# Performance work log

Measured on AMD Instinct MI355X. Metric: run time of the kernel, lower is better.

## Reference

```python
import jax, jax.numpy as jnp
import numpy as np

B, S, DIM = 4, 1024, 2048
N_HEAD, N_KV, HEAD_DIM = 32, 8, 64


def setup_inputs() -> dict:
    key = jax.random.key(0)
    k1, k2, k3, k4 = jax.random.split(key, 4)
    x = jax.random.normal(k1, (B, S, DIM), dtype=jnp.float32)
    # rotary table: [S, head_dim//2, 2] = (cos, sin)
    inv_freq = 1.0 / (10000.0 ** (jnp.arange(0, HEAD_DIM, 2, dtype=jnp.float32) / HEAD_DIM))
    t = jnp.arange(S, dtype=jnp.float32)
    ang = t[:, None] * inv_freq[None, :]
    freqs_cis = jnp.stack([jnp.cos(ang), jnp.sin(ang)], axis=-1)
    mask = jnp.tril(jnp.ones((S, S), dtype=bool))[None, None]  # causal bool [1,1,S,S]
    scale = 0.02
    wqkv = jax.random.normal(k2, ((N_HEAD + 2 * N_KV) * HEAD_DIM, DIM), dtype=jnp.float32) * scale
    wo = jax.random.normal(k3, (DIM, DIM), dtype=jnp.float32) * scale
    return {"x": x, "freqs_cis": freqs_cis, "mask": mask, "wqkv": wqkv, "wo": wo}


def _apply_rotary(x, freqs_cis):
    # x: [b, s, h, d]; freqs_cis: [s, d//2, 2]
    b, s, h, d = x.shape
    xr = x.reshape(b, s, h, d // 2, 2)
    fc = freqs_cis.reshape(1, s, 1, d // 2, 2)
    cos, sin = fc[..., 0], fc[..., 1]
    x0, x1 = xr[..., 0], xr[..., 1]
    out = jnp.stack([x0 * cos - x1 * sin, x1 * cos + x0 * sin], axis=-1)
    return out.reshape(b, s, h, d)


def reference(x, freqs_cis, mask, wqkv, wo):
    b, s, _ = x.shape
    qkv = jnp.einsum('bsd,ed->bse', x, wqkv)
    q, k, v = jnp.split(qkv, [N_HEAD * HEAD_DIM, (N_HEAD + N_KV) * HEAD_DIM], axis=-1)
    q = q.reshape(b, s, N_HEAD, HEAD_DIM)
    k = k.reshape(b, s, N_KV, HEAD_DIM)
    v = v.reshape(b, s, N_KV, HEAD_DIM)
    q = _apply_rotary(q, freqs_cis)
    k = _apply_rotary(k, freqs_cis)
    # [b, h, s, d]
    q = q.transpose(0, 2, 1, 3)
    k = k.transpose(0, 2, 1, 3)
    v = v.transpose(0, 2, 1, 3)
    g = N_HEAD // N_KV
    k = jnp.repeat(k, g, axis=1)
    v = jnp.repeat(v, g, axis=1)
    scale = 1.0 / np.sqrt(HEAD_DIM).astype(np.float32)
    scores = jnp.einsum('bhqd,bhkd->bhqk', q, k) * scale
    scores = jnp.where(mask, scores, jnp.float32(-jnp.inf))
    attn = jax.nn.softmax(scores, axis=-1)
    y = jnp.einsum('bhqk,bhkd->bhqd', attn, v)
    y = y.transpose(0, 2, 1, 3).reshape(b, s, DIM)
    return jnp.einsum('bsd,ed->bse', y, wo)
```

## Files before the change

kernel.cpp:

```cpp
#include <hip/hip_runtime.h>
#include <stdint.h>

typedef __bf16 bf16;
typedef __attribute__((ext_vector_type(8))) __bf16 bf16x8;
typedef __attribute__((ext_vector_type(4))) __bf16 bf16x4;
typedef __attribute__((ext_vector_type(4))) float f32x4;
typedef __attribute__((ext_vector_type(16))) float f32x16;
typedef __attribute__((ext_vector_type(2))) unsigned u32x2;

#define AS1 __attribute__((address_space(1)))
#define AS3 __attribute__((address_space(3)))

#if __has_builtin(__builtin_amdgcn_permlane32_swap)
#define HAVE_PLSWAP 1
#else
#define HAVE_PLSWAP 0
#endif

__device__ __forceinline__ float ex2(float x) {
#if __has_builtin(__builtin_amdgcn_exp2f)
  return __builtin_amdgcn_exp2f(x);
#else
  return exp2f(x);
#endif
}

__device__ __forceinline__ void barrier_f() {
  asm volatile("" ::: "memory");
  __builtin_amdgcn_s_barrier();
  asm volatile("" ::: "memory");
}

template <int N>
__device__ __forceinline__ void waitVm() {
  if constexpr (N == 0) asm volatile("s_waitcnt vmcnt(0)" ::: "memory");
  else if constexpr (N == 1) asm volatile("s_waitcnt vmcnt(1)" ::: "memory");
  else if constexpr (N == 2) asm volatile("s_waitcnt vmcnt(2)" ::: "memory");
  else if constexpr (N == 4) asm volatile("s_waitcnt vmcnt(4)" ::: "memory");
  else if constexpr (N == 6) asm volatile("s_waitcnt vmcnt(6)" ::: "memory");
  else static_assert(N == 0, "unsupported vmcnt");
  __builtin_amdgcn_sched_barrier(0);
}

__device__ __forceinline__ u32x2 swap32(uint32_t a, uint32_t b, int hh) {
#if HAVE_PLSWAP
  (void)hh;
  return __builtin_amdgcn_permlane32_swap(a, b, false, false);
#else
  u32x2 r;
  r[0] = hh ? __shfl_xor(b, 32) : a;
  r[1] = hh ? b : __shfl_xor(a, 32);
  return r;
#endif
}

template <int K>
__device__ __forceinline__ void relay_body(const float* __restrict__ W,
                                           bf16* __restrict__ Bp, int t) {
  const int off = t * 8;
  const int sub = (off & 511) >> 3;
  const int n = sub & 15, khi = sub >> 4;
  const int blk = off >> 9;
  const int kblk = blk & ((K >> 5) - 1);
  const int nblk = blk >> (31 - __builtin_clz(K >> 5));
  const float* src = W + (size_t)(nblk * 16 + n) * K + kblk * 32 + khi * 8;
  float4 a = *reinterpret_cast<const float4*>(src);
  float4 b = *reinterpret_cast<const float4*>(src + 4);
  bf16x8 o = { (bf16)a.x, (bf16)a.y, (bf16)a.z, (bf16)a.w,
               (bf16)b.x, (bf16)b.y, (bf16)b.z, (bf16)b.w };
  *reinterpret_cast<bf16x8*>(Bp + off) = o;
}

__global__ __launch_bounds__(256) void prologue_kernel(
    const float* __restrict__ x, bf16* __restrict__ xb,
    const float* __restrict__ wqkv, bf16* __restrict__ BpQ,
    const float* __restrict__ wo, bf16* __restrict__ BpO) {
  const int blk = blockIdx.x;
  if (blk < 8192) {
    const int i = blk * 256 + threadIdx.x;
    float4 v = reinterpret_cast<const float4*>(x)[i];
    bf16x4 r = { (bf16)v.x, (bf16)v.y, (bf16)v.z, (bf16)v.w };
    reinterpret_cast<bf16x4*>(xb)[i] = r;
  } else if (blk < 11264) {
    relay_body<2048>(wqkv, BpQ, (blk - 8192) * 256 + threadIdx.x);
  } else {
    relay_body<2048>(wo, BpO, (blk - 11264) * 256 + threadIdx.x);
  }
}

template <int BN, typename OutT, bool FUSE>
__global__ __launch_bounds__(512, 4) void gemmfc2(const bf16* __restrict__ A,
                                                  const bf16* __restrict__ Bp,
                                                  OutT* __restrict__ C,
                                                  const float* __restrict__ fc,
                                                  bf16* __restrict__ Qd,
                                                  bf16* __restrict__ Kd,
                                                  bf16* __restrict__ Vd,
                                                  int N, int K) {
  constexpr int WTN = BN / 8;
  constexpr int NR = WTN / 16;
  constexpr int NBF = 2 * NR;
  constexpr int ABUF = 64 * 128;
  __shared__ char smem[2 * ABUF];
  AS3 char* sm3 = (AS3 char*)smem;

  const int tid = threadIdx.x;
  const int w = tid >> 6, lane = tid & 63;
  const int fr = lane & 15, fq = lane >> 4;
  const int xorA = (fr & 7) << 4;

  const int orig = blockIdx.x;
  const int cpx = (int)gridDim.x >> 3;
  const int wgid = (orig & 7) * cpx + (orig >> 3);
  const int bm = (wgid & 63) * 64;
  const int bn = (wgid >> 6) * BN;
  const int KB = K >> 5;
  const int nbBase = (bn >> 4) + w * NR;

  f32x4 acc[4][NR] = {};

  auto stageA = [&](int t, int buf) {
    AS3 char* db = sm3 + buf * ABUF;
    const int row = tid >> 3;
    const int kslot = (tid & 7) ^ (row & 7);
    __builtin_amdgcn_global_load_lds(
        (const AS1 void*)(A + (size_t)(bm + row) * K + t * 64 + kslot * 8),
        (AS3 void*)(db + w * 1024), 16, 0, 0);
  };

  stageA(0, 0);

  const int NT = K >> 6;
  for (int t = 0; t < NT; ++t) {
    const int cb = t & 1;
    const bool pf = (t + 1 < NT);
    bf16x8 bF[NR][2];
#pragma unroll
    for (int ni = 0; ni < NR; ++ni)
#pragma unroll
      for (int ks = 0; ks < 2; ++ks)
        bF[ni][ks] = *reinterpret_cast<const bf16x8*>(
            Bp + ((size_t)(nbBase + ni) * KB + t * 2 + ks) * 512 + lane * 8);
    waitVm<NBF>();
    barrier_f();
    if (pf) stageA(t + 1, cb ^ 1);
    const char* cbA = smem + cb * ABUF;
    bf16x8 aF[2][2];
#pragma unroll
    for (int mi = 0; mi < 2; ++mi)
#pragma unroll
      for (int ks = 0; ks < 2; ++ks)
        aF[mi][ks] = *reinterpret_cast<const bf16x8*>(
            cbA + (mi * 16 + fr) * 128 + ((ks * 64 + fq * 16) ^ xorA));
    if (pf) waitVm<1>(); else waitVm<0>();
#pragma unroll
    for (int mp = 0; mp < 2; ++mp) {
      if (mp > 0) {
#pragma unroll
        for (int mi = 0; mi < 2; ++mi)
#pragma unroll
          for (int ks = 0; ks < 2; ++ks)
            aF[mi][ks] = *reinterpret_cast<const bf16x8*>(
                cbA + (32 + mi * 16 + fr) * 128 + ((ks * 64 + fq * 16) ^ xorA));
      }
      __builtin_amdgcn_s_setprio(1);
#pragma unroll
      for (int ks = 0; ks < 2; ++ks)
#pragma unroll
        for (int mi = 0; mi < 2; ++mi)
#pragma unroll
          for (int ni = 0; ni < NR; ++ni)
            acc[mp * 2 + mi][ni] = __builtin_amdgcn_mfma_f32_16x16x32_bf16(
                aF[mi][ks], bF[ni][ks], acc[mp * 2 + mi][ni], 0, 0, 0);
      __builtin_amdgcn_s_setprio(0);
    }
  }

  if constexpr (FUSE) {
    barrier_f();
    float* smF = (float*)smem;
    {
      const float* fsrc = fc + (size_t)(bm & 1023) * 64;
#pragma unroll
      for (int k = 0; k < 2; ++k)
        reinterpret_cast<float4*>(smF)[tid + k * 512] =
            reinterpret_cast<const float4*>(fsrc)[tid + k * 512];
    }
    __syncthreads();
    const float QSCALE = 0.125f * 1.4426950408889634f;
    const int par = fr & 1;
#pragma unroll
    for (int ni = 0; ni < NR; ++ni) {
      const int col = bn + w * WTN + ni * 16 + fr;
#pragma unroll
      for (int mi = 0; mi < 4; ++mi) {
        const int sl = mi * 16 + fq * 4;
        const int row0 = bm + sl;
        const int bb = row0 >> 10, s0 = row0 & 1023;
        if (col < 2560) {
          const int e = (col < 2048) ? col : col - 2048;
          const int d = e & 63, hq = e >> 6;
          const int dbase = d & ~1;
          bf16* dst = (col < 2048)
              ? Qd + (((size_t)(bb * 32 + hq)) * 1024 + s0) * 64 + d
              : Kd + (((size_t)(bb * 8 + hq)) * 1024 + s0) * 64 + d;
#pragma unroll
          for (int j = 0; j < 4; ++j) {
            float v = acc[mi][ni][j];
            float pv = __shfl_xor(v, 1);
            float2 csn = *reinterpret_cast<const float2*>(
                &smF[(sl + j) * 64 + dbase]);
            float r = par ? (v * csn.x + pv * csn.y)
                          : (v * csn.x - pv * csn.y);
            if (col < 2048) r *= QSCALE;
            dst[(size_t)j * 64] = (bf16)r;
          }
        } else {
          const int e = col - 2560, d = e & 63, hv = e >> 6;
          bf16x4 pk4;
#pragma unroll
          for (int j = 0; j < 4; ++j) pk4[j] = (bf16)acc[mi][ni][j];
          *reinterpret_cast<bf16x4*>(
              Vd + (((size_t)(bb * 8 + hv)) * 64 + d) * 1024 + s0) = pk4;
        }
      }
    }
  } else {
    const int cbn = bn + w * WTN + fr;
#pragma unroll
    for (int mi = 0; mi < 4; ++mi) {
      const int rb = bm + mi * 16 + fq * 4;
#pragma unroll
      for (int ni = 0; ni < NR; ++ni)
#pragma unroll
        for (int j = 0; j < 4; ++j)
          C[(size_t)(rb + j) * N + cbn + ni * 16] = (OutT)acc[mi][ni][j];
    }
  }
}

__global__ __launch_bounds__(512, 4) void attn_kernel(const bf16* __restrict__ Q,
                                                      const bf16* __restrict__ K,
                                                      const bf16* __restrict__ Vt,
                                                      bf16* __restrict__ Y) {
  __shared__ bf16 smem[18432];
  char* sb = (char*)smem;
  AS3 bf16* sA = (AS3 bf16*)smem;

  const int fid = blockIdx.x;
  const int hkv = fid & 7;
  const int hl = (fid >> 3) & 3;
  const int b = (fid >> 5) & 3;
  const int qq = (fid >> 7) & 3;
  const int q = (qq < 2) ? qq : 5 - qq;
  const int h = hkv * 4 + hl;

  const int w = threadIdx.x >> 6, lane = threadIdx.x & 63;
  const int qn = lane & 31;
  const int hh = lane >> 5;
  const int myqt = 2 * q + (w >> 2);
  const int q0 = myqt * 128 + (w & 3) * 32;
  const int mynch = 2 * myqt + 2;
  const int nchBlk = 4 * q + 4;
  const int maskFrom = q0 >> 6;
  const bf16* qbase = Q + (((size_t)(b * 32 + h)) * 1024 + q0) * 64;
  const char* kB = (const char*)(K + ((size_t)(b * 8 + hkv)) * 65536);
  const char* vB = (const char*)(Vt + ((size_t)(b * 8 + hkv)) * 65536);

  const int srow = lane >> 3;
  const int scb = (((lane & 7) ^ (lane >> 3)) << 4);
  const int xsw = (qn & 7) << 4;

  bf16x8 qf[4];
#pragma unroll
  for (int s = 0; s < 4; ++s)
    qf[s] = *reinterpret_cast<const bf16x8*>(&qbase[qn * 64 + s * 16 + hh * 8]);

  auto stage = [&](int ci, int buf) {
    const int kc = ci << 6;
    const int bo = buf * 4096;
    const int row = 8 * w + srow;
    __builtin_amdgcn_global_load_lds(
        (const AS1 void*)(kB + (size_t)(kc + row) * 128 + scb),
        (AS3 void*)(sA + bo + w * 512), 16, 0, 0);
    __builtin_amdgcn_global_load_lds(
        (const AS1 void*)(vB + (size_t)row * 2048 + kc * 2 + scb),
        (AS3 void*)(sA + 8192 + bo + w * 512), 16, 0, 0);
  };

  auto applyMask = [&](f32x16* st, int kc, int qg) {
#pragma unroll
    for (int mt = 0; mt < 2; ++mt)
#pragma unroll
      for (int r = 0; r < 16; ++r) {
        int kv = kc + mt * 32 + (r & 3) + 8 * (r >> 2) + 4 * hh;
        if (kv > qg) st[mt][r] = -3e38f;
      }
  };

  union F32U { float f; uint32_t u; };

  f32x16 O[2] = {};
  float mrow = -3e38f, lrow = 0.f;

  stage(0, 0);

  for (int ci = 0; ci < nchBlk; ++ci) {
    const int cur = ci & 1;
    const int kc = ci << 6;
    const bool pf = (ci + 1 < nchBlk);
    if (pf) stage(ci + 1, cur ^ 1);
    if (pf) waitVm<2>(); else waitVm<0>();
    barrier_f();
    const char* Kc = sb + cur * 8192;
    const char* Vc = sb + 16384 + cur * 8192;
    if (ci < mynch) {
      bf16x8 kf[2][4];
#pragma unroll
      for (int mt = 0; mt < 2; ++mt)
#pragma unroll
        for (int s = 0; s < 4; ++s)
          kf[mt][s] = *reinterpret_cast<const bf16x8*>(
              Kc + (qn + 32 * mt) * 128 + ((32 * s + 16 * hh) ^ xsw));
      f32x16 st[2] = {};
#pragma unroll
      for (int mt = 0; mt < 2; ++mt)
#pragma unroll
        for (int s = 0; s < 4; ++s)
          st[mt] = __builtin_amdgcn_mfma_f32_32x32x16_bf16(kf[mt][s], qf[s], st[mt], 0, 0, 0);
      if (ci >= maskFrom) applyMask(st, kc, q0 + qn);
      float t16[16];
#pragma unroll
      for (int i = 0; i < 16; ++i) t16[i] = fmaxf(st[0][i], st[1][i]);
#pragma unroll
      for (int off = 8; off >= 1; off >>= 1)
#pragma unroll
        for (int i = 0; i < off; ++i) t16[i] = fmaxf(t16[i], t16[i + off]);
      F32U fm; fm.f = t16[0];
      u32x2 rm = swap32(fm.u, fm.u, hh);
      F32U m0, m1; m0.u = rm[0]; m1.u = rm[1];
      float mx = fmaxf(m0.f, m1.f);
      if (!__all(mx - mrow <= 8.f)) {
        float mnew = fmaxf(mrow, mx);
        float alpha = ex2(mrow - mnew);
        lrow *= alpha;
#pragma unroll
        for (int dt = 0; dt < 2; ++dt)
#pragma unroll
          for (int r = 0; r < 16; ++r) O[dt][r] *= alpha;
        mrow = mnew;
      }
      union W { uint32_t u; bf16 b[2]; };
      W pk[2][8];
      float ps[16];
#pragma unroll
      for (int t = 0; t < 2; ++t)
#pragma unroll
        for (int wi = 0; wi < 8; ++wi) {
          float p0 = ex2(st[t][2 * wi] - mrow);
          float p1 = ex2(st[t][2 * wi + 1] - mrow);
          ps[t * 8 + wi] = p0 + p1;
          pk[t][wi].b[0] = (bf16)p0;
          pk[t][wi].b[1] = (bf16)p1;
        }
#pragma unroll
      for (int off = 8; off >= 1; off >>= 1)
#pragma unroll
        for (int i = 0; i < off; ++i) ps[i] += ps[i + off];
      F32U fs; fs.f = ps[0];
      u32x2 rs = swap32(fs.u, fs.u, hh);
      F32U s0, s1; s0.u = rs[0]; s1.u = rs[1];
      lrow += s0.f + s1.f;
#pragma unroll
      for (int s = 0; s < 4; ++s) {
        const int t = s >> 1, a0 = 4 * (s & 1);
        u32x2 rA = swap32(pk[t][a0 + 0].u, pk[t][a0 + 2].u, hh);
        u32x2 rB = swap32(pk[t][a0 + 1].u, pk[t][a0 + 3].u, hh);
        union BF { uint32_t u[4]; bf16x8 v; } bfrag;
        bfrag.u[0] = rA[0];
        bfrag.u[1] = rB[0];
        bfrag.u[2] = rA[1];
        bfrag.u[3] = rB[1];
#pragma unroll
        for (int dt = 0; dt < 2; ++dt) {
          bf16x8 vf = *reinterpret_cast<const bf16x8*>(
              Vc + (qn + 32 * dt) * 128 + ((32 * s + 16 * hh) ^ xsw));
          O[dt] = __builtin_amdgcn_mfma_f32_32x32x16_bf16(vf, bfrag.v, O[dt], 0, 0, 0);
        }
      }
    }
    barrier_f();
  }

  float inv = 1.f / lrow;
  bf16* Ytw = smem + w * 2304;
#pragma unroll
  for (int dt = 0; dt < 2; ++dt)
#pragma unroll
    for (int r = 0; r < 16; ++r) {
      int d = dt * 32 + (r & 3) + 8 * (r >> 2) + 4 * hh;
      Ytw[qn * 72 + d] = (bf16)(O[dt][r] * inv);
    }
  __syncthreads();
  const int qr = lane >> 1, c0 = (lane & 1) * 32;
  bf16* yout = Y + ((size_t)(b * 1024 + q0 + qr)) * 2048 + h * 64 + c0;
#pragma unroll
  for (int i = 0; i < 4; ++i)
    *reinterpret_cast<bf16x8*>(&yout[i * 8]) =
        *reinterpret_cast<const bf16x8*>(&Ytw[qr * 72 + c0 + i * 8]);
}

extern "C" void kernel_launch(void* const* d_in, const int* in_sizes, int n_in,
                              void* d_out, int out_size, void* d_ws, size_t ws_size,
                              hipStream_t stream) {
  const float* x    = (const float*)d_in[0];
  const float* fc   = (const float*)d_in[1];
  const float* wqkv = (const float*)d_in[3];
  const float* wo   = (const float*)d_in[4];
  float* out = (float*)d_out;

  char* ws = (char*)d_ws;
  const size_t MB = 1u << 20;
  bf16* xb    = (bf16*)(ws);
  bf16* BpQ   = (bf16*)(ws + 16 * MB);
  bf16* BpO   = (bf16*)(ws + 28 * MB);
  bf16* Qr    = (bf16*)(ws + 60 * MB);
  bf16* Kr    = (bf16*)(ws + 76 * MB);
  bf16* Vt    = (bf16*)(ws + 80 * MB);
  bf16* Y     = (bf16*)(ws + 84 * MB);

  prologue_kernel<<<13312, 256, 0, stream>>>(x, xb, wqkv, BpQ, wo, BpO);

  gemmfc2<384, bf16, true><<<512, 512, 0, stream>>>(
      xb, BpQ, (bf16*)nullptr, fc, Qr, Kr, Vt, 3072, 2048);

  attn_kernel<<<512, 512, 0, stream>>>(Qr, Kr, Vt, Y);

  gemmfc2<256, float, false><<<512, 512, 0, stream>>>(
      Y, BpO, out, nullptr, nullptr, nullptr, nullptr, 2048, 2048);
}
```

Before: 154.0 us.

## Restructure causal attention to process paired q-tiles sequentially per 4-wave block

Each attention block now has 4 waves instead of 8. It handles two 128-row query tiles, j and 7-j, one after the other, so every block does the same 18 KV chunks. Before, 8 waves shared staged chunks and waves whose tile was already done sat idle through the remaining chunks. The new layout removes that idle time inside a block and loads KV chunks in 64-row pieces with two loads per wave. The cost is less parallelism per block, a larger LDS footprint, and an epilogue that uses only a wave-local wait instead of a block barrier.

```diff
diff --git a/kernel.cpp b/kernel.cpp
--- a/kernel.cpp
+++ b/kernel.cpp
@@ -239,53 +239,48 @@
   }
 }
 
-__global__ __launch_bounds__(512, 4) void attn_kernel(const bf16* __restrict__ Q,
+__global__ __launch_bounds__(256, 4) void attn_kernel(const bf16* __restrict__ Q,
                                                       const bf16* __restrict__ K,
                                                       const bf16* __restrict__ Vt,
                                                       bf16* __restrict__ Y) {
-  __shared__ bf16 smem[18432];
+  __shared__ bf16 smem[25600];
   char* sb = (char*)smem;
-  AS3 bf16* sA = (AS3 bf16*)smem;
+  AS3 char* sA = (AS3 char*)smem;
 
   const int fid = blockIdx.x;
   const int hkv = fid & 7;
   const int hl = (fid >> 3) & 3;
   const int b = (fid >> 5) & 3;
-  const int qq = (fid >> 7) & 3;
-  const int q = (qq < 2) ? qq : 5 - qq;
+  const int j = (fid >> 7) & 3;
   const int h = hkv * 4 + hl;
 
   const int w = threadIdx.x >> 6, lane = threadIdx.x & 63;
   const int qn = lane & 31;
   const int hh = lane >> 5;
-  const int myqt = 2 * q + (w >> 2);
-  const int q0 = myqt * 128 + (w & 3) * 32;
-  const int mynch = 2 * myqt + 2;
-  const int nchBlk = 4 * q + 4;
-  const int maskFrom = q0 >> 6;
-  const bf16* qbase = Q + (((size_t)(b * 32 + h)) * 1024 + q0) * 64;
+  const int srow = lane >> 3;
+  const int scb = (((lane & 7) ^ srow) << 4);
+  const int xsw = (qn & 7) << 4;
+
+  const bf16* Qh = Q + ((size_t)(b * 32 + h)) * 65536;
   const char* kB = (const char*)(K + ((size_t)(b * 8 + hkv)) * 65536);
   const char* vB = (const char*)(Vt + ((size_t)(b * 8 + hkv)) * 65536);
 
-  const int srow = lane >> 3;
-  const int scb = (((lane & 7) ^ (lane >> 3)) << 4);
-  const int xsw = (qn & 7) << 4;
-
-  bf16x8 qf[4];
-#pragma unroll
-  for (int s = 0; s < 4; ++s)
-    qf[s] = *reinterpret_cast<const bf16x8*>(&qbase[qn * 64 + s * 16 + hh * 8]);
+  const int nchA = 2 * j + 2;
+  const int TOT = 18;
 
   auto stage = [&](int ci, int buf) {
     const int kc = ci << 6;
-    const int bo = buf * 4096;
-    const int row = 8 * w + srow;
-    __builtin_amdgcn_global_load_lds(
-        (const AS1 void*)(kB + (size_t)(kc + row) * 128 + scb),
-        (AS3 void*)(sA + bo + w * 512), 16, 0, 0);
-    __builtin_amdgcn_global_load_lds(
-        (const AS1 void*)(vB + (size_t)row * 2048 + kc * 2 + scb),
-        (AS3 void*)(sA + 8192 + bo + w * 512), 16, 0, 0);
+    const int bo = buf * 8192;
+#pragma unroll
+    for (int i = 0; i < 2; ++i) {
+      const int row = i * 32 + 8 * w + srow;
+      __builtin_amdgcn_global_load_lds(
+          (const AS1 void*)(kB + (size_t)(kc + row) * 128 + scb),
+          (AS3 void*)(sA + bo + i * 4096 + w * 1024), 16, 0, 0);
+      __builtin_amdgcn_global_load_lds(
+          (const AS1 void*)(vB + (size_t)row * 2048 + kc * 2 + scb),
+          (AS3 void*)(sA + 16384 + bo + i * 4096 + w * 1024), 16, 0, 0);
+    }
   };
 
   auto applyMask = [&](f32x16* st, int kc, int qg) {
@@ -299,115 +294,149 @@
   };
 
   union F32U { float f; uint32_t u; };
-
+  union W64 { uint32_t u; bf16 b[2]; };
+
+  int tq0 = j * 128 + w * 32;
+  int maskFrom = tq0 >> 6;
+  bf16x8 qf[4];
+#pragma unroll
+  for (int s = 0; s < 4; ++s)
+    qf[s] = *reinterpret_cast<const bf16x8*>(
+        &Qh[(size_t)(tq0 + qn) * 64 + s * 16 + hh * 8]);
   f32x16 O[2] = {};
   float mrow = -3e38f, lrow = 0.f;
 
+  auto epilogue = [&]() {
+    float inv = 1.f / lrow;
+    bf16* Ytw = smem + 16384 + w * 2304;
+#pragma unroll
+    for (int dt = 0; dt < 2; ++dt)
+#pragma unroll
+      for (int r = 0; r < 16; ++r) {
+        int d = dt * 32 + (r & 3) + 8 * (r >> 2) + 4 * hh;
+        Ytw[qn * 72 + d] = (bf16)(O[dt][r] * inv);
+      }
+    asm volatile("s_waitcnt lgkmcnt(0)" ::: "memory");
+    const int qr = lane >> 1, c0 = (lane & 1) * 32;
+    bf16* yout = Y + ((size_t)(b * 1024 + tq0 - w * 32 + (w * 32) + qr)) * 2048 + h * 64 + c0;
+#pragma unroll
+    for (int i = 0; i < 4; ++i)
+      *reinterpret_cast<bf16x8*>(&yout[i * 8]) =
+          *reinterpret_cast<const bf16x8*>(&Ytw[qr * 72 + c0 + i * 8]);
+  };
+
   stage(0, 0);
 
-  for (int ci = 0; ci < nchBlk; ++ci) {
-    const int cur = ci & 1;
-    const int kc = ci << 6;
-    const bool pf = (ci + 1 < nchBlk);
-    if (pf) stage(ci + 1, cur ^ 1);
-    if (pf) waitVm<2>(); else waitVm<0>();
+  for (int s = 0; s < TOT; ++s) {
+    const int cur = s & 1;
+    const int c = (s < nchA) ? s : s - nchA;
+    if (s + 1 < TOT) {
+      stage((s + 1 < nchA) ? s + 1 : s + 1 - nchA, cur ^ 1);
+      waitVm<4>();
+    } else {
+      waitVm<0>();
+    }
     barrier_f();
+    const int kc = c << 6;
     const char* Kc = sb + cur * 8192;
     const char* Vc = sb + 16384 + cur * 8192;
-    if (ci < mynch) {
-      bf16x8 kf[2][4];
-#pragma unroll
-      for (int mt = 0; mt < 2; ++mt)
-#pragma unroll
-        for (int s = 0; s < 4; ++s)
-          kf[mt][s] = *reinterpret_cast<const bf16x8*>(
-              Kc + (qn + 32 * mt) * 128 + ((32 * s + 16 * hh) ^ xsw));
-      f32x16 st[2] = {};
-#pragma unroll
-      for (int mt = 0; mt < 2; ++mt)
-#pragma unroll
-        for (int s = 0; s < 4; ++s)
-          st[mt] = __builtin_amdgcn_mfma_f32_32x32x16_bf16(kf[mt][s], qf[s], st[mt], 0, 0, 0);
-      if (ci >= maskFrom) applyMask(st, kc, q0 + qn);
-      float t16[16];
-#pragma unroll
-      for (int i = 0; i < 16; ++i) t16[i] = fmaxf(st[0][i], st[1][i]);
-#pragma unroll
-      for (int off = 8; off >= 1; off >>= 1)
-#pragma unroll
-        for (int i = 0; i < off; ++i) t16[i] = fmaxf(t16[i], t16[i + off]);
-      F32U fm; fm.f = t16[0];
-      u32x2 rm = swap32(fm.u, fm.u, hh);
-      F32U m0, m1; m0.u = rm[0]; m1.u = rm[1];
-      float mx = fmaxf(m0.f, m1.f);
-      if (!__all(mx - mrow <= 8.f)) {
-        float mnew = fmaxf(mrow, mx);
-        float alpha = ex2(mrow - mnew);
-        lrow *= alpha;
-#pragma unroll
-        for (int dt = 0; dt < 2; ++dt)
-#pragma unroll
-          for (int r = 0; r < 16; ++r) O[dt][r] *= alpha;
-        mrow = mnew;
-      }
-      union W { uint32_t u; bf16 b[2]; };
-      W pk[2][8];
-      float ps[16];
-#pragma unroll
-      for (int t = 0; t < 2; ++t)
-#pragma unroll
-        for (int wi = 0; wi < 8; ++wi) {
-          float p0 = ex2(st[t][2 * wi] - mrow);
-          float p1 = ex2(st[t][2 * wi + 1] - mrow);
-          ps[t * 8 + wi] = p0 + p1;
-          pk[t][wi].b[0] = (bf16)p0;
-          pk[t][wi].b[1] = (bf16)p1;
-        }
-#pragma unroll
-      for (int off = 8; off >= 1; off >>= 1)
-#pragma unroll
-        for (int i = 0; i < off; ++i) ps[i] += ps[i + off];
-      F32U fs; fs.f = ps[0];
-      u32x2 rs = swap32(fs.u, fs.u, hh);
-      F32U s0, s1; s0.u = rs[0]; s1.u = rs[1];
-      lrow += s0.f + s1.f;
-#pragma unroll
-      for (int s = 0; s < 4; ++s) {
-        const int t = s >> 1, a0 = 4 * (s & 1);
-        u32x2 rA = swap32(pk[t][a0 + 0].u, pk[t][a0 + 2].u, hh);
-        u32x2 rB = swap32(pk[t][a0 + 1].u, pk[t][a0 + 3].u, hh);
-        union BF { uint32_t u[4]; bf16x8 v; } bfrag;
-        bfrag.u[0] = rA[0];
-        bfrag.u[1] = rB[0];
-        bfrag.u[2] = rA[1];
-        bfrag.u[3] = rB[1];
-#pragma unroll
-        for (int dt = 0; dt < 2; ++dt) {
-          bf16x8 vf = *reinterpret_cast<const bf16x8*>(
-              Vc + (qn + 32 * dt) * 128 + ((32 * s + 16 * hh) ^ xsw));
-          O[dt] = __builtin_amdgcn_mfma_f32_32x32x16_bf16(vf, bfrag.v, O[dt], 0, 0, 0);
-        }
+
+    bf16x8 kf[2][4];
+#pragma unroll
+    for (int mt = 0; mt < 2; ++mt)
+#pragma unroll
+      for (int si = 0; si < 4; ++si)
+        kf[mt][si] = *reinterpret_cast<const bf16x8*>(
+            Kc + (qn + 32 * mt) * 128 + ((32 * si + 16 * hh) ^ xsw));
+    f32x16 st[2] = {};
+#pragma unroll
+    for (int mt = 0; mt < 2; ++mt)
+#pragma unroll
+      for (int si = 0; si < 4; ++si)
+        st[mt] = __builtin_amdgcn_mfma_f32_32x32x16_bf16(kf[mt][si], qf[si], st[mt], 0, 0, 0);
+    if (c >= maskFrom) applyMask(st, kc, tq0 + qn);
+    float t16[16];
+#pragma unroll
+    for (int i = 0; i < 16; ++i) t16[i] = fmaxf(st[0][i], st[1][i]);
+#pragma unroll
+    for (int off = 8; off >= 1; off >>= 1)
+#pragma unroll
+      for (int i = 0; i < off; ++i) t16[i] = fmaxf(t16[i], t16[i + off]);
+    F32U fm; fm.f = t16[0];
+    u32x2 rm = swap32(fm.u, fm.u, hh);
+    F32U m0, m1; m0.u = rm[0]; m1.u = rm[1];
+    float mx = fmaxf(m0.f, m1.f);
+    if (!__all(mx - mrow <= 8.f)) {
+      float mnew = fmaxf(mrow, mx);
+      float alpha = ex2(mrow - mnew);
+      lrow *= alpha;
+#pragma unroll
+      for (int dt = 0; dt < 2; ++dt)
+#pragma unroll
+        for (int r = 0; r < 16; ++r) O[dt][r] *= alpha;
+      mrow = mnew;
+    }
+    W64 pk[2][8];
+    float ps[16];
+#pragma unroll
+    for (int t = 0; t < 2; ++t)
+#pragma unroll
+      for (int wi = 0; wi < 8; ++wi) {
+        float p0 = ex2(st[t][2 * wi] - mrow);
+        float p1 = ex2(st[t][2 * wi + 1] - mrow);
+        ps[t * 8 + wi] = p0 + p1;
+        pk[t][wi].b[0] = (bf16)p0;
+        pk[t][wi].b[1] = (bf16)p1;
+      }
+#pragma unroll
+    for (int off = 8; off >= 1; off >>= 1)
+#pragma unroll
+      for (int i = 0; i < off; ++i) ps[i] += ps[i + off];
+    F32U fs; fs.f = ps[0];
+    u32x2 rs = swap32(fs.u, fs.u, hh);
+    F32U s0, s1; s0.u = rs[0]; s1.u = rs[1];
+    lrow += s0.f + s1.f;
+#pragma unroll
+    for (int si = 0; si < 4; ++si) {
+      const int t = si >> 1, a0 = 4 * (si & 1);
+      u32x2 rA = swap32(pk[t][a0 + 0].u, pk[t][a0 + 2].u, hh);
+      u32x2 rB = swap32(pk[t][a0 + 1].u, pk[t][a0 + 3].u, hh);
+      union BF { uint32_t u[4]; bf16x8 v; } bfrag;
+      bfrag.u[0] = rA[0];
+      bfrag.u[1] = rB[0];
+      bfrag.u[2] = rA[1];
+      bfrag.u[3] = rB[1];
+#pragma unroll
+      for (int dt = 0; dt < 2; ++dt) {
+        bf16x8 vf = *reinterpret_cast<const bf16x8*>(
+            Vc + (qn + 32 * dt) * 128 + ((32 * si + 16 * hh) ^ xsw));
+        O[dt] = __builtin_amdgcn_mfma_f32_32x32x16_bf16(vf, bfrag.v, O[dt], 0, 0, 0);
       }
     }
     barrier_f();
+
+    if (s == nchA - 1) {
+      const int nq0 = (7 - j) * 128 + w * 32;
+      bf16x8 nqf[4];
+#pragma unroll
+      for (int si = 0; si < 4; ++si)
+        nqf[si] = *reinterpret_cast<const bf16x8*>(
+            &Qh[(size_t)(nq0 + qn) * 64 + si * 16 + hh * 8]);
+      epilogue();
+      tq0 = nq0;
+      maskFrom = tq0 >> 6;
+#pragma unroll
+      for (int si = 0; si < 4; ++si) qf[si] = nqf[si];
+#pragma unroll
+      for (int dt = 0; dt < 2; ++dt)
+#pragma unroll
+        for (int r = 0; r < 16; ++r) O[dt][r] = 0.f;
+      mrow = -3e38f;
+      lrow = 0.f;
+    }
   }
 
-  float inv = 1.f / lrow;
-  bf16* Ytw = smem + w * 2304;
-#pragma unroll
-  for (int dt = 0; dt < 2; ++dt)
-#pragma unroll
-    for (int r = 0; r < 16; ++r) {
-      int d = dt * 32 + (r & 3) + 8 * (r >> 2) + 4 * hh;
-      Ytw[qn * 72 + d] = (bf16)(O[dt][r] * inv);
-    }
-  __syncthreads();
-  const int qr = lane >> 1, c0 = (lane & 1) * 32;
-  bf16* yout = Y + ((size_t)(b * 1024 + q0 + qr)) * 2048 + h * 64 + c0;
-#pragma unroll
-  for (int i = 0; i < 4; ++i)
-    *reinterpret_cast<bf16x8*>(&yout[i * 8]) =
-        *reinterpret_cast<const bf16x8*>(&Ytw[qr * 72 + c0 + i * 8]);
+  epilogue();
 }
 
 extern "C" void kernel_launch(void* const* d_in, const int* in_sizes, int n_in,
@@ -434,7 +463,7 @@
   gemmfc2<384, bf16, true><<<512, 512, 0, stream>>>(
       xb, BpQ, (bf16*)nullptr, fc, Qr, Kr, Vt, 3072, 2048);
 
-  attn_kernel<<<512, 512, 0, stream>>>(Qr, Kr, Vt, Y);
+  attn_kernel<<<512, 256, 0, stream>>>(Qr, Kr, Vt, Y);
 
   gemmfc2<256, float, false><<<512, 512, 0, stream>>>(
       Y, BpO, out, nullptr, nullptr, nullptr, nullptr, 2048, 2048);
```

After: 145.6 us. 1.06x faster.
